# Kernel tuning notes

Hardware: AMD Instinct MI355X
Metric: run time of the kernel (lower is better)

Reference implementation:

```python
import jax, jax.numpy as jnp
import numpy as np

VEC_SIZE = 1024
N_HEADS = 16
HEAD_SIZE = VEC_SIZE // N_HEADS


def setup_inputs() -> dict:
    key = jax.random.key(0)
    k1, k2, k3 = jax.random.split(key, 3)
    x = jax.random.normal(k1, (4, 2048, VEC_SIZE), dtype=jnp.float32)
    # nn.Linear weights stored as [out, in]; we apply as x @ W.T, so store transposed [in, out]
    w_qkv = jax.random.normal(k2, (VEC_SIZE, 3 * VEC_SIZE), dtype=jnp.float32) * (1.0 / np.sqrt(VEC_SIZE))
    w_out = jax.random.normal(k3, (VEC_SIZE, VEC_SIZE), dtype=jnp.float32) * (1.0 / np.sqrt(VEC_SIZE))
    return {"x": x, "w_qkv": w_qkv, "w_out": w_out}


def reference(x, w_qkv, w_out):
    batch, seq_len, _ = x.shape
    qkv = x @ w_qkv                                   # [B, S, 3*D]
    q, k, v = jnp.split(qkv, 3, axis=-1)
    def heads(m):
        return m.reshape(batch, seq_len, N_HEADS, HEAD_SIZE).transpose(0, 2, 1, 3)  # [B,H,S,d]
    q, k, v = heads(q), heads(k), heads(v)
    scale = 1.0 / np.sqrt(HEAD_SIZE).astype(np.float32)
    scores = jnp.einsum('bhqd,bhkd->bhqk', q, k) * scale        # [B,H,S,S]
    causal = jnp.tril(jnp.ones((seq_len, seq_len), dtype=bool))
    scores = jnp.where(causal[None, None], scores, jnp.finfo(scores.dtype).min)
    probs = jax.nn.softmax(scores, axis=-1)
    attn = jnp.einsum('bhqk,bhkd->bhqd', probs, v)              # [B,H,S,d]
    attn = attn.transpose(0, 2, 1, 3).reshape(batch, seq_len, VEC_SIZE)
    return attn @ w_out
```

## Files before the change

### kernel.cpp

```cpp
#include <hip/hip_runtime.h>
#include <float.h>


#define SEQ   2048
#define DIM   1024
#define NH    16
#define HD    64
#define MROWS 8192
#define BHTOT 64

#define PREP_CAST_BLOCKS  8192
#define PREP_WQKV_BLOCKS  3072
#define PREP_WOUT_BLOCKS  1024

typedef __bf16 bf16_t;
typedef __bf16 bf16x4 __attribute__((ext_vector_type(4)));
typedef __bf16 bf16x8 __attribute__((ext_vector_type(8)));
typedef float  f32x4  __attribute__((ext_vector_type(4)));

typedef const __attribute__((address_space(1))) unsigned int* gas_ptr;
typedef __attribute__((address_space(3))) unsigned int* las_ptr;

__device__ __forceinline__ void gll16(const bf16_t* g, bf16_t* l) {
    __builtin_amdgcn_global_load_lds((gas_ptr)g, (las_ptr)l, 16, 0, 0);
}

__global__ __launch_bounds__(256) void prep_kernel(
    const float* __restrict__ x,     bf16_t* __restrict__ xb,
    const float* __restrict__ w_qkv, bf16_t* __restrict__ wqkvT,
    const float* __restrict__ w_out, bf16_t* __restrict__ woutT)
{
    __shared__ float t[32][33];
    const int blk = blockIdx.x;

    if (blk < PREP_CAST_BLOCKS) {
        int i = (blk * 256 + threadIdx.x) * 4;
        float4 v = *(const float4*)(x + i);
        bf16x4 o = { (bf16_t)v.x, (bf16_t)v.y, (bf16_t)v.z, (bf16_t)v.w };
        *(bf16x4*)(xb + i) = o;
        return;
    }

    const float* w;  bf16_t* wT;  int N, tile;
    if (blk < PREP_CAST_BLOCKS + PREP_WQKV_BLOCKS) {
        tile = blk - PREP_CAST_BLOCKS;  w = w_qkv;  wT = wqkvT;  N = 3 * DIM;
    } else {
        tile = blk - PREP_CAST_BLOCKS - PREP_WQKV_BLOCKS;  w = w_out;  wT = woutT;  N = DIM;
    }
    const int bk = (tile & 31) * 32;
    const int bn = (tile >> 5) * 32;
    const int r = threadIdx.x >> 5, c = threadIdx.x & 31;
    #pragma unroll
    for (int i = 0; i < 4; i++)
        t[r + i * 8][c] = w[(size_t)(bk + r + i * 8) * N + bn + c];
    __syncthreads();
    #pragma unroll
    for (int i = 0; i < 4; i++)
        wT[(size_t)(bn + r + i * 8) * DIM + bk + c] = (bf16_t)t[c][r + i * 8];
}

__device__ __forceinline__ void gemm_dbuf_compute(
    const bf16_t* __restrict__ Ag, const bf16_t* __restrict__ Bg,
    int bm, int bn, bf16_t* As, bf16_t* Bs, f32x4 (&acc)[4][4])
{
    const int tid = threadIdx.x;
    const int lane = tid & 63, w = tid >> 6;
    const int quad = lane >> 4, l16 = lane & 15;
    const int wr = w >> 1, wc = w & 1;

    auto stage = [&](int kt, int buf) {
        const int k0 = kt * 64;
        bf16_t* Ad = As + buf * (128 * 64);
        bf16_t* Bd = Bs + buf * (128 * 64);
        #pragma unroll
        for (int p = 0; p < 4; p++) {
            int flat = p * 256 + tid;
            int row = flat >> 3, g = flat & 7, gs = g ^ (row & 7);
            gll16(Ag + (size_t)(bm + row) * DIM + k0 + gs * 8,
                  Ad + (size_t)(p * 256 + w * 64) * 8);
            gll16(Bg + (size_t)(bn + row) * DIM + k0 + gs * 8,
                  Bd + (size_t)(p * 256 + w * 64) * 8);
        }
    };

    stage(0, 0);
    __syncthreads();

    #pragma unroll 1
    for (int kt = 0; kt < 16; kt++) {
        const int cur = kt & 1;
        if (kt < 15) stage(kt + 1, cur ^ 1);
        const bf16_t* Ac = As + cur * (128 * 64);
        const bf16_t* Bc = Bs + cur * (128 * 64);
        #pragma unroll
        for (int ks = 0; ks < 2; ks++) {
            bf16x8 af[4], bfv[4];
            #pragma unroll
            for (int mt = 0; mt < 4; mt++) {
                int row = wr * 64 + mt * 16 + l16;
                int g = (ks * 4 + quad) ^ (row & 7);
                af[mt] = *(const bf16x8*)(Ac + row * 64 + g * 8);
            }
            #pragma unroll
            for (int nt = 0; nt < 4; nt++) {
                int row = wc * 64 + nt * 16 + l16;
                int g = (ks * 4 + quad) ^ (row & 7);
                bfv[nt] = *(const bf16x8*)(Bc + row * 64 + g * 8);
            }
            __builtin_amdgcn_s_setprio(1);
            #pragma unroll
            for (int mt = 0; mt < 4; mt++)
                #pragma unroll
                for (int nt = 0; nt < 4; nt++)
                    acc[mt][nt] = __builtin_amdgcn_mfma_f32_16x16x32_bf16(
                        af[mt], bfv[nt], acc[mt][nt], 0, 0, 0);
            __builtin_amdgcn_s_setprio(0);
        }
        __syncthreads();
    }
}

__global__ __launch_bounds__(256) void gemm_qkv_kernel(
    const bf16_t* __restrict__ Ag,
    const bf16_t* __restrict__ Bg,
    bf16_t* __restrict__ qN, bf16_t* __restrict__ kN, bf16_t* __restrict__ vT)
{
    __shared__ __align__(16) bf16_t As[2 * 128 * 64];
    __shared__ __align__(16) bf16_t Bs[2 * 128 * 64];
    const int tid = threadIdx.x;
    const int lane = tid & 63, w = tid >> 6;
    const int quad = lane >> 4, l16 = lane & 15;
    const int wr = w >> 1, wc = w & 1;
    const int bm = blockIdx.x * 128, bn = blockIdx.y * 128;

    f32x4 acc[4][4] = {};
    gemm_dbuf_compute(Ag, Bg, bm, bn, As, Bs, acc);

    const int which = bn >> 10;
    if (which == 2) {
        #pragma unroll
        for (int mt = 0; mt < 4; mt++)
            #pragma unroll
            for (int nt = 0; nt < 4; nt++) {
                int row0 = bm + wr * 64 + mt * 16 + quad * 4;
                int b = row0 >> 11, s0 = row0 & 2047;
                int col = bn + wc * 64 + nt * 16 + l16;
                int nn = col & 1023, h = nn >> 6, d = nn & 63;
                int bh = b * NH + h;
                bf16x4 vv;
                #pragma unroll
                for (int r = 0; r < 4; r++) vv[r] = (bf16_t)acc[mt][nt][r];
                *(bf16x4*)(vT + ((size_t)bh * HD + d) * SEQ + s0) = vv;
            }
    } else {
        const float qsc = (which == 0) ? 0.18033688011112042f : 1.0f;
        bf16_t* dst = (which == 0) ? qN : kN;
        #pragma unroll
        for (int mt = 0; mt < 4; mt++)
            #pragma unroll
            for (int nt = 0; nt < 4; nt++)
                #pragma unroll
                for (int r = 0; r < 4; r++) {
                    int row = bm + wr * 64 + mt * 16 + quad * 4 + r;
                    int b = row >> 11, s = row & 2047;
                    int col = bn + wc * 64 + nt * 16 + l16;
                    int nn = col & 1023, h = nn >> 6, d = nn & 63;
                    int bh = b * NH + h;
                    dst[((size_t)bh * SEQ + s) * HD + d] = (bf16_t)(acc[mt][nt][r] * qsc);
                }
    }
}

__global__ __launch_bounds__(256) void gemm_out_kernel(
    const bf16_t* __restrict__ Ag,
    const bf16_t* __restrict__ Bg,
    float* __restrict__ out)
{
    __shared__ __align__(16) bf16_t As[2 * 128 * 64];
    __shared__ __align__(16) bf16_t Bs[2 * 128 * 64];
    const int tid = threadIdx.x;
    const int lane = tid & 63, w = tid >> 6;
    const int quad = lane >> 4, l16 = lane & 15;
    const int wr = w >> 1, wc = w & 1;
    const int bm = blockIdx.x * 128, bn = blockIdx.y * 128;

    f32x4 acc[4][4] = {};
    gemm_dbuf_compute(Ag, Bg, bm, bn, As, Bs, acc);

    #pragma unroll
    for (int mt = 0; mt < 4; mt++)
        #pragma unroll
        for (int nt = 0; nt < 4; nt++)
            #pragma unroll
            for (int r = 0; r < 4; r++) {
                int row = bm + wr * 64 + mt * 16 + quad * 4 + r;
                int col = bn + wc * 64 + nt * 16 + l16;
                out[(size_t)row * DIM + col] = acc[mt][nt][r];
            }
}

__global__ __launch_bounds__(256) void attn_kernel(
    const bf16_t* __restrict__ qN, const bf16_t* __restrict__ kN,
    const bf16_t* __restrict__ vT, bf16_t* __restrict__ attnb)
{
    __shared__ __align__(16) char smem[40960];
    bf16_t* QPs = (bf16_t*)smem;
    bf16_t* Ks  = (bf16_t*)(smem + 8192);
    bf16_t* Vs  = (bf16_t*)(smem + 24576);

    const int bh = blockIdx.x;
    const int pr = blockIdx.y;
    const int tid = threadIdx.x;
    const int lane = tid & 63, w = tid >> 6;
    const int quad = lane >> 4, l16 = lane & 15;

    const bf16_t* qbase = qN + (size_t)bh * SEQ * HD;
    const bf16_t* kbase = kN + (size_t)bh * SEQ * HD;
    const bf16_t* vbase = vT + (size_t)bh * HD * SEQ;
    const int b = bh >> 4, h = bh & 15;

    auto stage_kv = [&](int kt, int buf) {
        bf16_t* Kd = Ks + buf * 4096;
        bf16_t* Vd = Vs + buf * 4096;
        #pragma unroll
        for (int p = 0; p < 2; p++) {
            int flat = p * 256 + tid;
            int row = flat >> 3, g = flat & 7;
            int gs = g ^ (row & 7);
            gll16(kbase + (size_t)(kt * 64 + row) * HD + gs * 8, Kd + (size_t)(p * 256 + w * 64) * 8);
            gll16(vbase + (size_t)row * SEQ + kt * 64 + gs * 8,  Vd + (size_t)(p * 256 + w * 64) * 8);
        }
    };

    #pragma unroll 1
    for (int phase = 0; phase < 2; phase++) {
        const int t = (phase == 0) ? pr : 31 - pr;

        __syncthreads();
        #pragma unroll
        for (int p = 0; p < 2; p++) {
            int flat = p * 256 + tid;
            int row = flat >> 3, g = flat & 7;
            int gs = g ^ (row & 7);
            gll16(qbase + (size_t)(t * 64 + row) * HD + gs * 8,
                  QPs + (size_t)(p * 256 + w * 64) * 8);
        }
        stage_kv(0, 0);
        __syncthreads();

        bf16x8 qa[2];
        #pragma unroll
        for (int ks = 0; ks < 2; ks++) {
            int row = w * 16 + l16;
            int g = (ks * 4 + quad) ^ (row & 7);
            qa[ks] = *(const bf16x8*)(QPs + row * 64 + g * 8);
        }

        f32x4 o[4] = {};
        float l_part = 0.0f;

        const int rl = w * 16 + l16;
        const int qrow = t * 64 + rl;

        for (int kt = 0; kt <= t; kt++) {
            const int cur = kt & 1;
            if (kt < t) stage_kv(kt + 1, cur ^ 1);

            const bf16_t* Kc = Ks + cur * 4096;
            const bf16_t* Vc = Vs + cur * 4096;

            f32x4 s[4] = {};
            #pragma unroll
            for (int ks = 0; ks < 2; ks++) {
                bf16x8 kb[4];
                #pragma unroll
                for (int nt = 0; nt < 4; nt++) {
                    int row = nt * 16 + l16;
                    int g = (ks * 4 + quad) ^ (row & 7);
                    kb[nt] = *(const bf16x8*)(Kc + row * 64 + g * 8);
                }
                __builtin_amdgcn_s_setprio(1);
                #pragma unroll
                for (int nt = 0; nt < 4; nt++)
                    s[nt] = __builtin_amdgcn_mfma_f32_16x16x32_bf16(
                        kb[nt], qa[ks], s[nt], 0, 0, 0);
                __builtin_amdgcn_s_setprio(0);
            }

            const bool maskit = (kt == t);
            #pragma unroll
            for (int nt = 0; nt < 4; nt++) {
                bf16x4 pk;
                #pragma unroll
                for (int r = 0; r < 4; r++) {
                    float pv;
                    if (maskit) {
                        int key = kt * 64 + nt * 16 + quad * 4 + r;
                        pv = (key <= qrow) ? __builtin_amdgcn_exp2f(s[nt][r]) : 0.0f;
                    } else {
                        pv = __builtin_amdgcn_exp2f(s[nt][r]);
                    }
                    l_part += pv;
                    pk[r] = (bf16_t)pv;
                }
                int gs = (nt * 2 + (quad >> 1)) ^ (rl & 7);
                *(bf16x4*)(QPs + rl * 64 + gs * 8 + (quad & 1) * 4) = pk;
            }

            #pragma unroll
            for (int ks = 0; ks < 2; ks++) {
                bf16x8 vb[4], pb;
                #pragma unroll
                for (int dt = 0; dt < 4; dt++) {
                    int row = dt * 16 + l16;
                    int g = (ks * 4 + quad) ^ (row & 7);
                    vb[dt] = *(const bf16x8*)(Vc + row * 64 + g * 8);
                }
                {
                    int g = (ks * 4 + quad) ^ (rl & 7);
                    pb = *(const bf16x8*)(QPs + rl * 64 + g * 8);
                }
                __builtin_amdgcn_s_setprio(1);
                #pragma unroll
                for (int dt = 0; dt < 4; dt++)
                    o[dt] = __builtin_amdgcn_mfma_f32_16x16x32_bf16(
                        vb[dt], pb, o[dt], 0, 0, 0);
                __builtin_amdgcn_s_setprio(0);
            }

            __syncthreads();
        }

        float lsum = l_part;
        lsum += __shfl_xor(lsum, 16, 64);
        lsum += __shfl_xor(lsum, 32, 64);
        float inv = 1.0f / lsum;
        const int srow = t * 64 + w * 16 + l16;
        #pragma unroll
        for (int dt = 0; dt < 4; dt++) {
            bf16x4 ov;
            #pragma unroll
            for (int r = 0; r < 4; r++) ov[r] = (bf16_t)(o[dt][r] * inv);
            *(bf16x4*)(attnb + ((size_t)(b * SEQ + srow)) * DIM + h * HD + dt * 16 + quad * 4) = ov;
        }
    }
}

extern "C" void kernel_launch(void* const* d_in, const int* in_sizes, int n_in,
                              void* d_out, int out_size, void* d_ws, size_t ws_size,
                              hipStream_t stream) {
    const float* x     = (const float*)d_in[0];
    const float* w_qkv = (const float*)d_in[1];
    const float* w_out = (const float*)d_in[2];
    float* out = (float*)d_out;

    bf16_t* xb    = (bf16_t*)d_ws;
    bf16_t* wqkvT = xb    + (size_t)MROWS * DIM;
    bf16_t* woutT = wqkvT + (size_t)3 * DIM * DIM;
    bf16_t* qNb   = woutT + (size_t)DIM * DIM;
    bf16_t* kNb   = qNb   + (size_t)BHTOT * SEQ * HD;
    bf16_t* vTb   = kNb   + (size_t)BHTOT * SEQ * HD;
    bf16_t* attnb = vTb   + (size_t)BHTOT * SEQ * HD;

    prep_kernel<<<PREP_CAST_BLOCKS + PREP_WQKV_BLOCKS + PREP_WOUT_BLOCKS, 256, 0, stream>>>(
        x, xb, w_qkv, wqkvT, w_out, woutT);
    gemm_qkv_kernel<<<dim3(MROWS / 128, 3 * DIM / 128), 256, 0, stream>>>(xb, wqkvT, qNb, kNb, vTb);
    attn_kernel<<<dim3(BHTOT, 16), 256, 0, stream>>>(qNb, kNb, vTb, attnb);
    gemm_out_kernel<<<dim3(MROWS / 128, DIM / 128), 256, 0, stream>>>(attnb, woutT, out);
}
```

Baseline: 228.8 us.

## Replace double-buffered GEMM LDS staging with single buffer

Both projection GEMMs drop double-buffered LDS staging for a single buffer, loading each K tile between two barriers before computing on it. This halves LDS use per block (64KB to 32KB), so more blocks may fit per CU and hide latency through occupancy. In exchange, the global-to-LDS prefetch no longer overlaps the MFMA work within a block, and there is an extra barrier per K step.

```diff
diff --git a/kernel.cpp b/kernel.cpp
--- a/kernel.cpp
+++ b/kernel.cpp
@@ -59,7 +59,7 @@
         wT[(size_t)(bn + r + i * 8) * DIM + bk + c] = (bf16_t)t[c][r + i * 8];
 }
 
-__device__ __forceinline__ void gemm_dbuf_compute(
+__device__ __forceinline__ void gemm_sbuf_compute(
     const bf16_t* __restrict__ Ag, const bf16_t* __restrict__ Bg,
     int bm, int bn, bf16_t* As, bf16_t* Bs, f32x4 (&acc)[4][4])
 {
@@ -68,30 +68,24 @@
     const int quad = lane >> 4, l16 = lane & 15;
     const int wr = w >> 1, wc = w & 1;
 
-    auto stage = [&](int kt, int buf) {
+    auto stage = [&](int kt) {
         const int k0 = kt * 64;
-        bf16_t* Ad = As + buf * (128 * 64);
-        bf16_t* Bd = Bs + buf * (128 * 64);
         #pragma unroll
         for (int p = 0; p < 4; p++) {
             int flat = p * 256 + tid;
             int row = flat >> 3, g = flat & 7, gs = g ^ (row & 7);
             gll16(Ag + (size_t)(bm + row) * DIM + k0 + gs * 8,
-                  Ad + (size_t)(p * 256 + w * 64) * 8);
+                  As + (size_t)(p * 256 + w * 64) * 8);
             gll16(Bg + (size_t)(bn + row) * DIM + k0 + gs * 8,
-                  Bd + (size_t)(p * 256 + w * 64) * 8);
+                  Bs + (size_t)(p * 256 + w * 64) * 8);
         }
     };
-
-    stage(0, 0);
-    __syncthreads();
 
     #pragma unroll 1
     for (int kt = 0; kt < 16; kt++) {
-        const int cur = kt & 1;
-        if (kt < 15) stage(kt + 1, cur ^ 1);
-        const bf16_t* Ac = As + cur * (128 * 64);
-        const bf16_t* Bc = Bs + cur * (128 * 64);
+        __syncthreads();
+        stage(kt);
+        __syncthreads();
         #pragma unroll
         for (int ks = 0; ks < 2; ks++) {
             bf16x8 af[4], bfv[4];
@@ -99,13 +93,13 @@
             for (int mt = 0; mt < 4; mt++) {
                 int row = wr * 64 + mt * 16 + l16;
                 int g = (ks * 4 + quad) ^ (row & 7);
-                af[mt] = *(const bf16x8*)(Ac + row * 64 + g * 8);
+                af[mt] = *(const bf16x8*)(As + row * 64 + g * 8);
             }
             #pragma unroll
             for (int nt = 0; nt < 4; nt++) {
                 int row = wc * 64 + nt * 16 + l16;
                 int g = (ks * 4 + quad) ^ (row & 7);
-                bfv[nt] = *(const bf16x8*)(Bc + row * 64 + g * 8);
+                bfv[nt] = *(const bf16x8*)(Bs + row * 64 + g * 8);
             }
             __builtin_amdgcn_s_setprio(1);
             #pragma unroll
@@ -116,7 +110,6 @@
                         af[mt], bfv[nt], acc[mt][nt], 0, 0, 0);
             __builtin_amdgcn_s_setprio(0);
         }
-        __syncthreads();
     }
 }
 
@@ -125,8 +118,8 @@
     const bf16_t* __restrict__ Bg,
     bf16_t* __restrict__ qN, bf16_t* __restrict__ kN, bf16_t* __restrict__ vT)
 {
-    __shared__ __align__(16) bf16_t As[2 * 128 * 64];
-    __shared__ __align__(16) bf16_t Bs[2 * 128 * 64];
+    __shared__ __align__(16) bf16_t As[128 * 64];
+    __shared__ __align__(16) bf16_t Bs[128 * 64];
     const int tid = threadIdx.x;
     const int lane = tid & 63, w = tid >> 6;
     const int quad = lane >> 4, l16 = lane & 15;
@@ -134,7 +127,7 @@
     const int bm = blockIdx.x * 128, bn = blockIdx.y * 128;
 
     f32x4 acc[4][4] = {};
-    gemm_dbuf_compute(Ag, Bg, bm, bn, As, Bs, acc);
+    gemm_sbuf_compute(Ag, Bg, bm, bn, As, Bs, acc);
 
     const int which = bn >> 10;
     if (which == 2) {
@@ -176,8 +169,8 @@
     const bf16_t* __restrict__ Bg,
     float* __restrict__ out)
 {
-    __shared__ __align__(16) bf16_t As[2 * 128 * 64];
-    __shared__ __align__(16) bf16_t Bs[2 * 128 * 64];
+    __shared__ __align__(16) bf16_t As[128 * 64];
+    __shared__ __align__(16) bf16_t Bs[128 * 64];
     const int tid = threadIdx.x;
     const int lane = tid & 63, w = tid >> 6;
     const int quad = lane >> 4, l16 = lane & 15;
@@ -185,7 +178,7 @@
     const int bm = blockIdx.x * 128, bn = blockIdx.y * 128;
 
     f32x4 acc[4][4] = {};
-    gemm_dbuf_compute(Ag, Bg, bm, bn, As, Bs, acc);
+    gemm_sbuf_compute(Ag, Bg, bm, bn, As, Bs, acc);
 
     #pragma unroll
     for (int mt = 0; mt < 4; mt++)
```

New measurement: 233.0 us, median of 3. Within noise of the previous version (+1.8%).
